# Optimization experiments

Hardware: AMD Instinct MI355X
Metric: run time of the kernel (lower is better)

## Reference

```python
import jax, jax.numpy as jnp
import numpy as np

M = 7          # window size
SHIFT = 3      # window_size // 2 (shift=True)
NUM_HEADS = 4


def _relative_position_index(m):
    coords = np.stack(np.meshgrid(np.arange(m), np.arange(m), indexing='ij')).reshape(2, -1)
    rel = (coords[:, :, None] - coords[:, None, :]).transpose(1, 2, 0).copy()  # (N,N,2)
    rel[..., 0] += m - 1
    rel[..., 1] += m - 1
    rel[..., 0] *= 2 * m - 1
    return rel.sum(-1).astype(np.int32)  # (N,N)


def _shift_attn_mask(H, W, m, s):
    img = np.zeros((H, W), np.float32)
    cnt = 0
    for hs in (slice(0, -m), slice(-m, -s), slice(-s, None)):
        for ws in (slice(0, -m), slice(-m, -s), slice(-s, None)):
            img[hs, ws] = cnt
            cnt += 1
    mw = img.reshape(H // m, m, W // m, m).transpose(0, 2, 1, 3).reshape(-1, m * m)  # (nW, N)
    diff = mw[:, None, :] - mw[:, :, None]
    return np.where(diff != 0, np.float32(-100.0), np.float32(0.0))  # (nW, N, N)


def setup_inputs():
    key = jax.random.key(0)
    k0, k1, k2, k3 = jax.random.split(key, 4)
    B, C, H, W = 32, 128, 112, 112
    h = NUM_HEADS
    x = jax.random.normal(k0, (B, C, H, W), jnp.float32)
    norm_w = jnp.ones((C,), jnp.float32)
    norm_b = jnp.zeros((C,), jnp.float32)
    qkv_w = jax.random.normal(k1, (3 * C, C), jnp.float32) * 0.02
    qkv_b = jnp.zeros((3 * C,), jnp.float32)
    proj_w = jax.random.normal(k2, (C, C), jnp.float32) * 0.02
    proj_b = jnp.zeros((C,), jnp.float32)
    bias_table = jax.random.normal(k3, ((2 * M - 1) ** 2, h), jnp.float32) * 0.02
    rel_index = jnp.asarray(_relative_position_index(M))
    attn_mask = jnp.asarray(_shift_attn_mask(H, W, M, SHIFT))
    return dict(x=x, norm_w=norm_w, norm_b=norm_b, qkv_w=qkv_w, qkv_b=qkv_b,
                proj_w=proj_w, proj_b=proj_b, bias_table=bias_table,
                rel_index=rel_index, attn_mask=attn_mask)


def reference(x, norm_w, norm_b, qkv_w, qkv_b, proj_w, proj_b, bias_table, rel_index, attn_mask):
    B, C, H, W = x.shape
    h = bias_table.shape[1]
    d = C // h
    N = M * M
    nH, nW = H // M, W // M

    xp = jnp.transpose(x, (0, 2, 3, 1))  # (B,H,W,C)
    shortcut = xp
    mu = xp.mean(-1, keepdims=True)
    var = ((xp - mu) ** 2).mean(-1, keepdims=True)
    xn = (xp - mu) / jnp.sqrt(var + 1e-5) * norm_w + norm_b

    xn = jnp.roll(xn, (-SHIFT, -SHIFT), (1, 2))  # cyclic shift

    # window partition -> (B*nH*nW, N, C)
    w = xn.reshape(B, nH, M, nW, M, C).transpose((0, 1, 3, 2, 4, 5)).reshape(-1, N, C)

    qkv = w @ qkv_w.T + qkv_b  # (B_, N, 3C)
    qkv = qkv.reshape(-1, N, 3, h, d).transpose((2, 0, 3, 1, 4))  # (3, B_, h, N, d)
    q, k, v = qkv[0], qkv[1], qkv[2]

    attn = jnp.einsum('bhnd,bhmd->bhnm', q, k) * (d ** -0.5)  # (B_, h, N, N)
    bias = bias_table[rel_index.reshape(-1)].reshape(N, N, h).transpose((2, 0, 1))  # (h,N,N)
    attn = attn + bias[None]

    nWnd = attn_mask.shape[0]  # number of windows per image
    attn = attn.reshape(B, nWnd, h, N, N) + attn_mask[None, :, None]
    attn = attn.reshape(-1, h, N, N)

    p = jax.nn.softmax(attn, axis=-1)
    o = jnp.einsum('bhnm,bhmd->bhnd', p, v).transpose((0, 2, 1, 3)).reshape(-1, N, C)
    o = o @ proj_w.T + proj_b

    # window reverse -> (B,H,W,C)
    o = o.reshape(B, nH, nW, M, M, C).transpose((0, 1, 3, 2, 4, 5)).reshape(B, H, W, C)
    o = jnp.roll(o, (SHIFT, SHIFT), (1, 2))  # reverse shift

    return jnp.transpose(shortcut + o, (0, 3, 1, 2))  # (B,C,H,W)
```

## Files before the change

### kernel.cpp

```cpp
#include <hip/hip_runtime.h>
#include <hip/hip_bf16.h>

typedef __attribute__((ext_vector_type(8))) short bf16x8;
typedef __attribute__((ext_vector_type(4))) float f32x4;
typedef __attribute__((ext_vector_type(8))) unsigned short ushort8;

__device__ __forceinline__ float bf2f(unsigned short u) {
  union { unsigned int i; float f; } v; v.i = ((unsigned int)u) << 16; return v.f;
}
__device__ __forceinline__ unsigned short f2bf(float f) {
  __hip_bfloat16 h = __float2bfloat16(f);
  unsigned short u; __builtin_memcpy(&u, &h, 2); return u;
}

__global__ void k_prep(const float* __restrict__ qkvw, const float* __restrict__ projw,
                       unsigned short* __restrict__ qkvw_bf,
                       unsigned short* __restrict__ projw_bf) {
  int t = blockIdx.x * 256 + threadIdx.x;
  int i = t * 4;
  const float* src;
  unsigned short* dst;
  int idx;
  if (i < 49152) { src = qkvw; dst = qkvw_bf; idx = i; }
  else           { src = projw; dst = projw_bf; idx = i - 49152; }
  float4 v = *(const float4*)(src + idx);
  union { unsigned short u[4]; uint2 v2; } o;
  o.u[0] = f2bf(v.x); o.u[1] = f2bf(v.y); o.u[2] = f2bf(v.z); o.u[3] = f2bf(v.w);
  *(uint2*)(dst + idx) = o.v2;
}

__global__ void k_bias(const float* __restrict__ bt,
                       const int* __restrict__ ri,
                       float* __restrict__ bp) {
  int t = blockIdx.x * 256 + threadIdx.x;
  int hq = t >> 12;
  int q  = (t >> 6) & 63;
  int k  = t & 63;
  float v = -1e30f;
  if (q < 49 && k < 49) v = bt[ri[q * 49 + k] * 4 + hq];
  bp[t] = v;
}

__global__ void k_mask(const float* __restrict__ am, float* __restrict__ mp) {
  int t = blockIdx.x * 256 + threadIdx.x;
  int w = t >> 12;
  int q = (t >> 6) & 63;
  int k = t & 63;
  float v = -1e30f;
  if (q < 49 && k < 49) v = am[w * 2401 + q * 49 + k];
  mp[t] = v;
}

__global__ __launch_bounds__(256, 3) void k_ln(const float* __restrict__ x,
                                               const float* __restrict__ nw,
                                               const float* __restrict__ nb,
                                               unsigned short* __restrict__ xw) {
  int p = blockIdx.x * 256 + threadIdx.x;
  int b = p / 12544;
  int r = p - b * 12544;
  int hh = r / 112;
  int wp = r - hh * 112;
  const float* bx = x + (size_t)b * 1605632 + r;

  float v[128];
  float s0 = 0.f, s1 = 0.f, q0 = 0.f, q1 = 0.f;
  #pragma unroll
  for (int c = 0; c < 128; c += 2) {
    float a = bx[(size_t)c * 12544];
    float bb = bx[(size_t)(c + 1) * 12544];
    v[c] = a; v[c + 1] = bb;
    s0 += a; q0 += a * a;
    s1 += bb; q1 += bb * bb;
  }
  float mu = (s0 + s1) * 0.0078125f;
  float var = (q0 + q1) * 0.0078125f - mu * mu;
  float rstd = rsqrtf(var + 1e-5f);

  int h2 = hh + 109; if (h2 >= 112) h2 -= 112;
  int w2 = wp + 109; if (w2 >= 112) w2 -= 112;
  int wh = h2 / 7, ii = h2 - wh * 7;
  int ww = w2 / 7, jj = w2 - ww * 7;
  int winl = (b * 16 + wh) * 16 + ww;
  unsigned short* dst = xw + ((size_t)winl * 49 + ii * 7 + jj) * 128;

  #pragma unroll
  for (int g = 0; g < 4; ++g) {
    unsigned int pk[16];
    #pragma unroll
    for (int q = 0; q < 16; ++q) {
      int c = g * 32 + 2 * q;
      float y0 = (v[c] - mu) * rstd * nw[c]         + nb[c];
      float y1 = (v[c + 1] - mu) * rstd * nw[c + 1] + nb[c + 1];
      pk[q] = (unsigned int)f2bf(y0) | ((unsigned int)f2bf(y1) << 16);
    }
    uint4* d4 = (uint4*)(dst + g * 32);
    #pragma unroll
    for (int k = 0; k < 4; ++k)
      d4[k] = make_uint4(pk[4 * k], pk[4 * k + 1], pk[4 * k + 2], pk[4 * k + 3]);
  }
}

__global__ __launch_bounds__(256, 3) void k_attn(
    const unsigned short* __restrict__ xw,
    const unsigned short* __restrict__ qkvw,
    const float* __restrict__ qkvb,
    const unsigned short* __restrict__ projw,
    const float* __restrict__ projb,
    const float* __restrict__ biasp,
    const float* __restrict__ maskp,
    unsigned short* __restrict__ yw) {
  __shared__ __attribute__((aligned(16))) char smem[49152];
  const int tid  = threadIdx.x;
  const int lane = tid & 63;
  const int h    = tid >> 6;
  const int m15  = lane & 15;
  const int quad = lane >> 4;
  const int win  = blockIdx.x;
  const int b    = win >> 8;
  const int wrem = win & 255;
  const int wh   = wrem >> 4;
  const int ww   = wrem & 15;
  const f32x4 fz = {0.f, 0.f, 0.f, 0.f};

  {
    const uint4* gsrc = (const uint4*)(xw + (size_t)win * 6272);
    #pragma unroll
    for (int it = 0; it < 4; ++it) {
      int cc = tid + it * 256;
      int row = cc >> 4, col = cc & 15;
      uint4 v = make_uint4(0u, 0u, 0u, 0u);
      if (cc < 784) v = gsrc[cc];
      *(uint4*)(smem + row * 256 + ((col ^ (row & 7)) << 4)) = v;
    }
  }
  __syncthreads();

  bf16x8 xf[4][4];
  #pragma unroll
  for (int mt = 0; mt < 4; ++mt) {
    int row = mt * 16 + m15;
    #pragma unroll
    for (int kt = 0; kt < 4; ++kt)
      xf[mt][kt] = *(const bf16x8*)(smem + row * 256 + (((kt * 4 + quad) ^ (row & 7)) << 4));
  }
  __syncthreads();

  char* const hb  = smem + h * 12288;
  char* const qpb = hb;
  char* const kpb = hb + 4096;
  char* const vpb = hb + 8192;

  #pragma unroll
  for (int g = 0; g < 2; ++g) {
    char* const dst = g ? kpb : qpb;
    #pragma unroll
    for (int sp = 0; sp < 2; ++sp) {
      int nt = g * 8 + 2 * h + sp;
      bf16x8 wfr[4];
      #pragma unroll
      for (int kt = 0; kt < 4; ++kt)
        wfr[kt] = *(const bf16x8*)(qkvw + (nt * 16 + m15) * 128 + kt * 32 + quad * 8);
      float4 b4 = *(const float4*)(qkvb + nt * 16 + quad * 4);
      #pragma unroll
      for (int mt = 0; mt < 4; ++mt) {
        f32x4 acc = fz;
        #pragma unroll
        for (int kt = 0; kt < 4; ++kt)
          acc = __builtin_amdgcn_mfma_f32_16x16x32_bf16(wfr[kt], xf[mt][kt], acc, 0, 0, 0);
        int row = mt * 16 + m15;
        union { unsigned short u[4]; uint2 v2; } o;
        o.u[0] = f2bf(acc[0] + b4.x); o.u[1] = f2bf(acc[1] + b4.y);
        o.u[2] = f2bf(acc[2] + b4.z); o.u[3] = f2bf(acc[3] + b4.w);
        int chunk = sp * 2 + (quad >> 1);
        *(uint2*)(dst + row * 64 + ((chunk ^ ((row >> 1) & 3)) << 4) + (quad & 1) * 8) = o.v2;
      }
    }
  }
  #pragma unroll
  for (int sp = 0; sp < 2; ++sp) {
    int nt = 16 + 2 * h + sp;
    bf16x8 wfr[4];
    #pragma unroll
    for (int kt = 0; kt < 4; ++kt)
      wfr[kt] = *(const bf16x8*)(qkvw + (nt * 16 + m15) * 128 + kt * 32 + quad * 8);
    float bias = qkvb[nt * 16 + m15];
    int dsub = sp * 16 + m15;
    #pragma unroll
    for (int mt = 0; mt < 4; ++mt) {
      f32x4 acc = fz;
      #pragma unroll
      for (int kt = 0; kt < 4; ++kt)
        acc = __builtin_amdgcn_mfma_f32_16x16x32_bf16(xf[mt][kt], wfr[kt], acc, 0, 0, 0);
      union { unsigned short u[4]; uint2 v2; } o;
      #pragma unroll
      for (int rr = 0; rr < 4; ++rr) o.u[rr] = f2bf(acc[rr] + bias);
      int chunk = mt * 2 + (quad >> 1);
      *(uint2*)(vpb + dsub * 128 + ((chunk ^ (dsub & 7)) << 4) + (quad & 1) * 8) = o.v2;
    }
  }

  bf16x8 qf[4], kf[4];
  #pragma unroll
  for (int t = 0; t < 4; ++t) {
    int row = t * 16 + m15;
    int sw = ((row >> 1) & 3) << 4;
    qf[t] = *(const bf16x8*)(qpb + row * 64 + ((quad << 4) ^ sw));
    kf[t] = *(const bf16x8*)(kpb + row * 64 + ((quad << 4) ^ sw));
  }
  f32x4 st[4][4];
  #pragma unroll
  for (int nt = 0; nt < 4; ++nt)
    #pragma unroll
    for (int mt = 0; mt < 4; ++mt)
      st[nt][mt] = __builtin_amdgcn_mfma_f32_16x16x32_bf16(kf[nt], qf[mt], fz, 0, 0, 0);

  const float* bp = biasp + h * 4096;
  const float* mp = maskp + wrem * 4096;
  #pragma unroll
  for (int mt = 0; mt < 4; ++mt) {
    int q = mt * 16 + m15;
    float sv[16];
    #pragma unroll
    for (int nt = 0; nt < 4; ++nt) {
      float4 bb = *(const float4*)(bp + q * 64 + nt * 16 + quad * 4);
      float4 mm = *(const float4*)(mp + q * 64 + nt * 16 + quad * 4);
      sv[nt * 4 + 0] = st[nt][mt][0] * 0.17677669529663687f + bb.x + mm.x;
      sv[nt * 4 + 1] = st[nt][mt][1] * 0.17677669529663687f + bb.y + mm.y;
      sv[nt * 4 + 2] = st[nt][mt][2] * 0.17677669529663687f + bb.z + mm.z;
      sv[nt * 4 + 3] = st[nt][mt][3] * 0.17677669529663687f + bb.w + mm.w;
    }
    float mx = sv[0];
    #pragma unroll
    for (int j = 1; j < 16; ++j) mx = fmaxf(mx, sv[j]);
    mx = fmaxf(mx, __shfl_xor(mx, 16));
    mx = fmaxf(mx, __shfl_xor(mx, 32));
    float sum = 0.f;
    #pragma unroll
    for (int j = 0; j < 16; ++j) { sv[j] = __expf(sv[j] - mx); sum += sv[j]; }
    sum += __shfl_xor(sum, 16);
    sum += __shfl_xor(sum, 32);
    float rinv = 1.0f / sum;
    #pragma unroll
    for (int nt = 0; nt < 4; ++nt) {
      union { unsigned short u[4]; uint2 v2; } o;
      #pragma unroll
      for (int rr = 0; rr < 4; ++rr) o.u[rr] = f2bf(sv[nt * 4 + rr] * rinv);
      int chunk = nt * 2 + (quad >> 1);
      *(uint2*)(qpb + q * 128 + ((chunk ^ (m15 & 7)) << 4) + (quad & 1) * 8) = o.v2;
    }
  }

  #pragma unroll
  for (int tt = 0; tt < 4; ++tt) {
    bf16x8 pf[2];
    #pragma unroll
    for (int kt = 0; kt < 2; ++kt) {
      int row = tt * 16 + m15;
      pf[kt] = *(const bf16x8*)(qpb + row * 128 + (((kt * 4 + quad) ^ (m15 & 7)) << 4));
    }
    #pragma unroll
    for (int dt = 0; dt < 2; ++dt) {
      f32x4 acc = fz;
      #pragma unroll
      for (int kt = 0; kt < 2; ++kt) {
        bf16x8 vf = *(const bf16x8*)(vpb + (dt * 16 + m15) * 128 + (((kt * 4 + quad) ^ (m15 & 7)) << 4));
        acc = __builtin_amdgcn_mfma_f32_16x16x32_bf16(vf, pf[kt], acc, 0, 0, 0);
      }
      int row = tt * 16 + m15;
      union { unsigned short u[4]; uint2 v2; } o;
      #pragma unroll
      for (int rr = 0; rr < 4; ++rr) o.u[rr] = f2bf(acc[rr]);
      int chunk = dt * 2 + (quad >> 1);
      *(uint2*)(qpb + row * 64 + ((chunk ^ ((row >> 1) & 3)) << 4) + (quad & 1) * 8) = o.v2;
    }
  }
  __syncthreads();

  bf16x8 of[4][4];
  #pragma unroll
  for (int mt = 0; mt < 4; ++mt) {
    int row = mt * 16 + m15;
    int sw = ((row >> 1) & 3) << 4;
    #pragma unroll
    for (int kt = 0; kt < 4; ++kt)
      of[mt][kt] = *(const bf16x8*)(smem + kt * 12288 + row * 64 + ((quad << 4) ^ sw));
  }
  int pixo[4];
  #pragma unroll
  for (int mt = 0; mt < 4; ++mt) {
    int token = mt * 16 + m15;
    int ii = token / 7, jj = token - ii * 7;
    int gh = wh * 7 + ii + 3; if (gh >= 112) gh -= 112;
    int gw = ww * 7 + jj + 3; if (gw >= 112) gw -= 112;
    pixo[mt] = gh * 112 + gw;
  }
  const size_t obase = (size_t)b * 1605632;
  #pragma unroll
  for (int sp = 0; sp < 2; ++sp) {
    int ct = 2 * h + sp;
    bf16x8 wf[4];
    #pragma unroll
    for (int kt = 0; kt < 4; ++kt)
      wf[kt] = *(const bf16x8*)(projw + (ct * 16 + m15) * 128 + kt * 32 + quad * 8);
    float4 pb4 = *(const float4*)(projb + ct * 16 + quad * 4);
    #pragma unroll
    for (int mt = 0; mt < 4; ++mt) {
      f32x4 acc = fz;
      #pragma unroll
      for (int kt = 0; kt < 4; ++kt)
        acc = __builtin_amdgcn_mfma_f32_16x16x32_bf16(wf[kt], of[mt][kt], acc, 0, 0, 0);
      int token = mt * 16 + m15;
      if (token < 49) {
        union { unsigned short u[4]; uint2 v2; } o;
        o.u[0] = f2bf(acc[0] + pb4.x); o.u[1] = f2bf(acc[1] + pb4.y);
        o.u[2] = f2bf(acc[2] + pb4.z); o.u[3] = f2bf(acc[3] + pb4.w);
        *(uint2*)(yw + obase + (size_t)pixo[mt] * 128 + ct * 16 + quad * 4) = o.v2;
      }
    }
  }
}

__global__ __launch_bounds__(256) void k_out(const unsigned short* __restrict__ yws,
                                             const float* __restrict__ x,
                                             float* __restrict__ out) {
  __shared__ __attribute__((aligned(16))) char T[28928];
  int tid = threadIdx.x;
  int bid = blockIdx.x;
  int b = bid / 112;
  int hh = bid - b * 112;
  const unsigned short* src = yws + (size_t)(b * 112 + hh) * 14336;
  #pragma unroll
  for (int it = 0; it < 7; ++it) {
    int cc = tid + it * 256;
    int w = cc >> 4, ci = cc & 15;
    *(uint4*)(T + ci * 1808 + w * 16) = *(const uint4*)(src + w * 128 + ci * 8);
  }
  __syncthreads();
  int c = tid >> 1, half = tid & 1;
  const char* tr = T + (c >> 3) * 1808 + (c & 7) * 2;
  size_t rowoff = ((size_t)(b * 128 + c) * 112 + hh) * 112;
  const float* xr = x + rowoff;
  float* outr = out + rowoff;
  #pragma unroll
  for (int s2 = 0; s2 < 7; ++s2) {
    int w = half * 56 + s2 * 8;
    float4 xa = *(const float4*)(xr + w);
    float4 xb = *(const float4*)(xr + w + 4);
    float4 oa, ob;
    oa.x = bf2f(*(const unsigned short*)(tr + (w + 0) * 16)) + xa.x;
    oa.y = bf2f(*(const unsigned short*)(tr + (w + 1) * 16)) + xa.y;
    oa.z = bf2f(*(const unsigned short*)(tr + (w + 2) * 16)) + xa.z;
    oa.w = bf2f(*(const unsigned short*)(tr + (w + 3) * 16)) + xa.w;
    ob.x = bf2f(*(const unsigned short*)(tr + (w + 4) * 16)) + xb.x;
    ob.y = bf2f(*(const unsigned short*)(tr + (w + 5) * 16)) + xb.y;
    ob.z = bf2f(*(const unsigned short*)(tr + (w + 6) * 16)) + xb.z;
    ob.w = bf2f(*(const unsigned short*)(tr + (w + 7) * 16)) + xb.w;
    *(float4*)(outr + w) = oa;
    *(float4*)(outr + w + 4) = ob;
  }
}

extern "C" void kernel_launch(void* const* d_in, const int* in_sizes, int n_in,
                              void* d_out, int out_size, void* d_ws, size_t ws_size,
                              hipStream_t stream) {
  const float* x     = (const float*)d_in[0];
  const float* nw    = (const float*)d_in[1];
  const float* nb    = (const float*)d_in[2];
  const float* qkvw  = (const float*)d_in[3];
  const float* qkvb  = (const float*)d_in[4];
  const float* projw = (const float*)d_in[5];
  const float* projb = (const float*)d_in[6];
  const float* bt    = (const float*)d_in[7];
  const int*   ri    = (const int*)d_in[8];
  const float* am    = (const float*)d_in[9];

  unsigned short* xw   = (unsigned short*)d_ws;
  unsigned short* yws  = (unsigned short*)((char*)d_ws + 102760448);
  float*          bp   = (float*)((char*)d_ws + 205520896);
  float*          mp   = (float*)((char*)d_ws + 205586432);
  unsigned short* qwbf = (unsigned short*)((char*)d_ws + 209780736);
  unsigned short* pwbf = (unsigned short*)((char*)d_ws + 209879040);
  float* out = (float*)d_out;

  k_prep<<<64,   256, 0, stream>>>(qkvw, projw, qwbf, pwbf);
  k_bias<<<64,   256, 0, stream>>>(bt, ri, bp);
  k_mask<<<4096, 256, 0, stream>>>(am, mp);
  k_ln  <<<1568, 256, 0, stream>>>(x, nw, nb, xw);
  k_attn<<<8192, 256, 0, stream>>>(xw, qwbf, qkvb, pwbf, projb, bp, mp, yws);
  k_out <<<3584, 256, 0, stream>>>(yws, x, out);
}
```

Before: 848.9 us.

## Keep Q/K/P in registers via 16x16x16 MFMA and shrink LDS footprint

New measurement: 891.8 us. +5.1%, slower.

```diff
diff --git a/kernel.cpp b/kernel.cpp
--- a/kernel.cpp
+++ b/kernel.cpp
@@ -2,6 +2,7 @@
 #include <hip/hip_bf16.h>
 
 typedef __attribute__((ext_vector_type(8))) short bf16x8;
+typedef __attribute__((ext_vector_type(4))) short bf16x4;
 typedef __attribute__((ext_vector_type(4))) float f32x4;
 typedef __attribute__((ext_vector_type(8))) unsigned short ushort8;
 
@@ -11,6 +12,19 @@
 __device__ __forceinline__ unsigned short f2bf(float f) {
   __hip_bfloat16 h = __float2bfloat16(f);
   unsigned short u; __builtin_memcpy(&u, &h, 2); return u;
+}
+__device__ __forceinline__ unsigned int pk2(float a, float b) {
+  return (unsigned int)f2bf(a) | ((unsigned int)f2bf(b) << 16);
+}
+
+__device__ __forceinline__ f32x4 mfma16(bf16x4 a, bf16x4 b, f32x4 c) {
+#if __has_builtin(__builtin_amdgcn_mfma_f32_16x16x16bf16_1k)
+  return __builtin_amdgcn_mfma_f32_16x16x16bf16_1k(a, b, c, 0, 0, 0);
+#else
+  asm volatile("v_mfma_f32_16x16x16_bf16 %0, %1, %2, %0\n\ts_nop 7\n\ts_nop 7"
+               : "+v"(c) : "v"(a), "v"(b));
+  return c;
+#endif
 }
 
 __global__ void k_prep(const float* __restrict__ qkvw, const float* __restrict__ projw,
@@ -51,7 +65,7 @@
   mp[t] = v;
 }
 
-__global__ __launch_bounds__(256, 3) void k_ln(const float* __restrict__ x,
+__global__ __launch_bounds__(256, 4) void k_ln(const float* __restrict__ x,
                                                const float* __restrict__ nw,
                                                const float* __restrict__ nb,
                                                unsigned short* __restrict__ xw) {
@@ -62,18 +76,14 @@
   int wp = r - hh * 112;
   const float* bx = x + (size_t)b * 1605632 + r;
 
-  float v[128];
-  float s0 = 0.f, s1 = 0.f, q0 = 0.f, q1 = 0.f;
-  #pragma unroll
-  for (int c = 0; c < 128; c += 2) {
-    float a = bx[(size_t)c * 12544];
-    float bb = bx[(size_t)(c + 1) * 12544];
-    v[c] = a; v[c + 1] = bb;
-    s0 += a; q0 += a * a;
-    s1 += bb; q1 += bb * bb;
-  }
-  float mu = (s0 + s1) * 0.0078125f;
-  float var = (q0 + q1) * 0.0078125f - mu * mu;
+  float sum = 0.f, ss = 0.f;
+  #pragma unroll 16
+  for (int c = 0; c < 128; ++c) {
+    float v = bx[(size_t)c * 12544];
+    sum += v; ss += v * v;
+  }
+  float mu = sum * 0.0078125f;
+  float var = ss * 0.0078125f - mu * mu;
   float rstd = rsqrtf(var + 1e-5f);
 
   int h2 = hh + 109; if (h2 >= 112) h2 -= 112;
@@ -89,8 +99,10 @@
     #pragma unroll
     for (int q = 0; q < 16; ++q) {
       int c = g * 32 + 2 * q;
-      float y0 = (v[c] - mu) * rstd * nw[c]         + nb[c];
-      float y1 = (v[c + 1] - mu) * rstd * nw[c + 1] + nb[c + 1];
+      float v0 = bx[(size_t)c * 12544];
+      float v1 = bx[(size_t)(c + 1) * 12544];
+      float y0 = (v0 - mu) * rstd * nw[c]     + nb[c];
+      float y1 = (v1 - mu) * rstd * nw[c + 1] + nb[c + 1];
       pk[q] = (unsigned int)f2bf(y0) | ((unsigned int)f2bf(y1) << 16);
     }
     uint4* d4 = (uint4*)(dst + g * 32);
@@ -100,7 +112,7 @@
   }
 }
 
-__global__ __launch_bounds__(256, 3) void k_attn(
+__global__ __launch_bounds__(256, 4) void k_attn(
     const unsigned short* __restrict__ xw,
     const unsigned short* __restrict__ qkvw,
     const float* __restrict__ qkvb,
@@ -109,7 +121,7 @@
     const float* __restrict__ biasp,
     const float* __restrict__ maskp,
     unsigned short* __restrict__ yw) {
-  __shared__ __attribute__((aligned(16))) char smem[49152];
+  __shared__ __attribute__((aligned(16))) char smem[32768];
   const int tid  = threadIdx.x;
   const int lane = tid & 63;
   const int h    = tid >> 6;
@@ -135,99 +147,85 @@
   }
   __syncthreads();
 
-  bf16x8 xf[4][4];
-  #pragma unroll
-  for (int mt = 0; mt < 4; ++mt) {
-    int row = mt * 16 + m15;
-    #pragma unroll
-    for (int kt = 0; kt < 4; ++kt)
-      xf[mt][kt] = *(const bf16x8*)(smem + row * 256 + (((kt * 4 + quad) ^ (row & 7)) << 4));
-  }
-  __syncthreads();
-
-  char* const hb  = smem + h * 12288;
-  char* const qpb = hb;
-  char* const kpb = hb + 4096;
-  char* const vpb = hb + 8192;
-
-  #pragma unroll
-  for (int g = 0; g < 2; ++g) {
-    char* const dst = g ? kpb : qpb;
+  char* const vpb = smem + 16384 + h * 4096;
+
+  bf16x4 qq[2][4], kk[2][4];
+  #pragma unroll
+  for (int mh = 0; mh < 2; ++mh) {
+    bf16x8 xf[2][4];
+    #pragma unroll
+    for (int m2 = 0; m2 < 2; ++m2) {
+      int row = (mh * 2 + m2) * 16 + m15;
+      #pragma unroll
+      for (int kt = 0; kt < 4; ++kt)
+        xf[m2][kt] = *(const bf16x8*)(smem + row * 256 + (((kt * 4 + quad) ^ (row & 7)) << 4));
+    }
+    #pragma unroll
+    for (int g = 0; g < 2; ++g) {
+      #pragma unroll
+      for (int sp = 0; sp < 2; ++sp) {
+        int nt = g * 8 + 2 * h + sp;
+        bf16x8 wfr[4];
+        #pragma unroll
+        for (int kt = 0; kt < 4; ++kt)
+          wfr[kt] = *(const bf16x8*)(qkvw + (nt * 16 + m15) * 128 + kt * 32 + quad * 8);
+        float4 b4 = *(const float4*)(qkvb + nt * 16 + quad * 4);
+        #pragma unroll
+        for (int m2 = 0; m2 < 2; ++m2) {
+          int mt = mh * 2 + m2;
+          f32x4 acc = fz;
+          #pragma unroll
+          for (int kt = 0; kt < 4; ++kt)
+            acc = __builtin_amdgcn_mfma_f32_16x16x32_bf16(wfr[kt], xf[m2][kt], acc, 0, 0, 0);
+          union { unsigned int u[2]; bf16x4 v; } pk;
+          pk.u[0] = pk2(acc[0] + b4.x, acc[1] + b4.y);
+          pk.u[1] = pk2(acc[2] + b4.z, acc[3] + b4.w);
+          if (g) kk[sp][mt] = pk.v; else qq[sp][mt] = pk.v;
+        }
+      }
+    }
     #pragma unroll
     for (int sp = 0; sp < 2; ++sp) {
-      int nt = g * 8 + 2 * h + sp;
+      int nt = 16 + 2 * h + sp;
       bf16x8 wfr[4];
       #pragma unroll
       for (int kt = 0; kt < 4; ++kt)
         wfr[kt] = *(const bf16x8*)(qkvw + (nt * 16 + m15) * 128 + kt * 32 + quad * 8);
-      float4 b4 = *(const float4*)(qkvb + nt * 16 + quad * 4);
-      #pragma unroll
-      for (int mt = 0; mt < 4; ++mt) {
+      float bias = qkvb[nt * 16 + m15];
+      int dsub = sp * 16 + m15;
+      #pragma unroll
+      for (int m2 = 0; m2 < 2; ++m2) {
+        int mt = mh * 2 + m2;
         f32x4 acc = fz;
         #pragma unroll
         for (int kt = 0; kt < 4; ++kt)
-          acc = __builtin_amdgcn_mfma_f32_16x16x32_bf16(wfr[kt], xf[mt][kt], acc, 0, 0, 0);
-        int row = mt * 16 + m15;
-        union { unsigned short u[4]; uint2 v2; } o;
-        o.u[0] = f2bf(acc[0] + b4.x); o.u[1] = f2bf(acc[1] + b4.y);
-        o.u[2] = f2bf(acc[2] + b4.z); o.u[3] = f2bf(acc[3] + b4.w);
-        int chunk = sp * 2 + (quad >> 1);
-        *(uint2*)(dst + row * 64 + ((chunk ^ ((row >> 1) & 3)) << 4) + (quad & 1) * 8) = o.v2;
+          acc = __builtin_amdgcn_mfma_f32_16x16x32_bf16(xf[m2][kt], wfr[kt], acc, 0, 0, 0);
+        uint2 o;
+        o.x = pk2(acc[0] + bias, acc[1] + bias);
+        o.y = pk2(acc[2] + bias, acc[3] + bias);
+        int chunk = mt * 2 + (quad >> 1);
+        *(uint2*)(vpb + dsub * 128 + ((chunk ^ (dsub & 7)) << 4) + (quad & 1) * 8) = o;
       }
     }
   }
-  #pragma unroll
-  for (int sp = 0; sp < 2; ++sp) {
-    int nt = 16 + 2 * h + sp;
-    bf16x8 wfr[4];
-    #pragma unroll
-    for (int kt = 0; kt < 4; ++kt)
-      wfr[kt] = *(const bf16x8*)(qkvw + (nt * 16 + m15) * 128 + kt * 32 + quad * 8);
-    float bias = qkvb[nt * 16 + m15];
-    int dsub = sp * 16 + m15;
-    #pragma unroll
-    for (int mt = 0; mt < 4; ++mt) {
-      f32x4 acc = fz;
-      #pragma unroll
-      for (int kt = 0; kt < 4; ++kt)
-        acc = __builtin_amdgcn_mfma_f32_16x16x32_bf16(xf[mt][kt], wfr[kt], acc, 0, 0, 0);
-      union { unsigned short u[4]; uint2 v2; } o;
-      #pragma unroll
-      for (int rr = 0; rr < 4; ++rr) o.u[rr] = f2bf(acc[rr] + bias);
-      int chunk = mt * 2 + (quad >> 1);
-      *(uint2*)(vpb + dsub * 128 + ((chunk ^ (dsub & 7)) << 4) + (quad & 1) * 8) = o.v2;
-    }
-  }
-
-  bf16x8 qf[4], kf[4];
-  #pragma unroll
-  for (int t = 0; t < 4; ++t) {
-    int row = t * 16 + m15;
-    int sw = ((row >> 1) & 3) << 4;
-    qf[t] = *(const bf16x8*)(qpb + row * 64 + ((quad << 4) ^ sw));
-    kf[t] = *(const bf16x8*)(kpb + row * 64 + ((quad << 4) ^ sw));
-  }
-  f32x4 st[4][4];
-  #pragma unroll
-  for (int nt = 0; nt < 4; ++nt)
-    #pragma unroll
-    for (int mt = 0; mt < 4; ++mt)
-      st[nt][mt] = __builtin_amdgcn_mfma_f32_16x16x32_bf16(kf[nt], qf[mt], fz, 0, 0, 0);
-
-  const float* bp = biasp + h * 4096;
-  const float* mp = maskp + wrem * 4096;
+
+  bf16x4 pp[4][4];
+  const float* bp_ = biasp + h * 4096;
+  const float* mp_ = maskp + wrem * 4096;
   #pragma unroll
   for (int mt = 0; mt < 4; ++mt) {
     int q = mt * 16 + m15;
     float sv[16];
     #pragma unroll
     for (int nt = 0; nt < 4; ++nt) {
-      float4 bb = *(const float4*)(bp + q * 64 + nt * 16 + quad * 4);
-      float4 mm = *(const float4*)(mp + q * 64 + nt * 16 + quad * 4);
-      sv[nt * 4 + 0] = st[nt][mt][0] * 0.17677669529663687f + bb.x + mm.x;
-      sv[nt * 4 + 1] = st[nt][mt][1] * 0.17677669529663687f + bb.y + mm.y;
-      sv[nt * 4 + 2] = st[nt][mt][2] * 0.17677669529663687f + bb.z + mm.z;
-      sv[nt * 4 + 3] = st[nt][mt][3] * 0.17677669529663687f + bb.w + mm.w;
+      f32x4 s = mfma16(kk[0][nt], qq[0][mt], fz);
+      s = mfma16(kk[1][nt], qq[1][mt], s);
+      float4 bb = *(const float4*)(bp_ + q * 64 + nt * 16 + quad * 4);
+      float4 mm = *(const float4*)(mp_ + q * 64 + nt * 16 + quad * 4);
+      sv[nt * 4 + 0] = s[0] * 0.17677669529663687f + bb.x + mm.x;
+      sv[nt * 4 + 1] = s[1] * 0.17677669529663687f + bb.y + mm.y;
+      sv[nt * 4 + 2] = s[2] * 0.17677669529663687f + bb.z + mm.z;
+      sv[nt * 4 + 3] = s[3] * 0.17677669529663687f + bb.w + mm.w;
     }
     float mx = sv[0];
     #pragma unroll
@@ -242,38 +240,45 @@
     float rinv = 1.0f / sum;
     #pragma unroll
     for (int nt = 0; nt < 4; ++nt) {
-      union { unsigned short u[4]; uint2 v2; } o;
-      #pragma unroll
-      for (int rr = 0; rr < 4; ++rr) o.u[rr] = f2bf(sv[nt * 4 + rr] * rinv);
-      int chunk = nt * 2 + (quad >> 1);
-      *(uint2*)(qpb + q * 128 + ((chunk ^ (m15 & 7)) << 4) + (quad & 1) * 8) = o.v2;
-    }
-  }
-
-  #pragma unroll
-  for (int tt = 0; tt < 4; ++tt) {
-    bf16x8 pf[2];
-    #pragma unroll
-    for (int kt = 0; kt < 2; ++kt) {
-      int row = tt * 16 + m15;
-      pf[kt] = *(const bf16x8*)(qpb + row * 128 + (((kt * 4 + quad) ^ (m15 & 7)) << 4));
-    }
+      union { unsigned int u[2]; bf16x4 v; } pk;
+      pk.u[0] = pk2(sv[nt * 4 + 0] * rinv, sv[nt * 4 + 1] * rinv);
+      pk.u[1] = pk2(sv[nt * 4 + 2] * rinv, sv[nt * 4 + 3] * rinv);
+      pp[mt][nt] = pk.v;
+    }
+  }
+
+  bf16x4 vf4[4][2];
+  #pragma unroll
+  for (int nt = 0; nt < 4; ++nt)
+    #pragma unroll
+    for (int dt = 0; dt < 2; ++dt) {
+      int r = dt * 16 + m15;
+      union { uint2 u; bf16x4 v; } ld;
+      ld.u = *(const uint2*)(vpb + r * 128 + (((nt * 2 + (quad >> 1)) ^ (r & 7)) << 4) + (quad & 1) * 8);
+      vf4[nt][dt] = ld.v;
+    }
+  f32x4 oacc[4][2];
+  #pragma unroll
+  for (int tt = 0; tt < 4; ++tt)
     #pragma unroll
     for (int dt = 0; dt < 2; ++dt) {
       f32x4 acc = fz;
       #pragma unroll
-      for (int kt = 0; kt < 2; ++kt) {
-        bf16x8 vf = *(const bf16x8*)(vpb + (dt * 16 + m15) * 128 + (((kt * 4 + quad) ^ (m15 & 7)) << 4));
-        acc = __builtin_amdgcn_mfma_f32_16x16x32_bf16(vf, pf[kt], acc, 0, 0, 0);
-      }
+      for (int nt = 0; nt < 4; ++nt)
+        acc = mfma16(vf4[nt][dt], pp[tt][nt], acc);
+      oacc[tt][dt] = acc;
+    }
+  #pragma unroll
+  for (int tt = 0; tt < 4; ++tt)
+    #pragma unroll
+    for (int dt = 0; dt < 2; ++dt) {
       int row = tt * 16 + m15;
-      union { unsigned short u[4]; uint2 v2; } o;
-      #pragma unroll
-      for (int rr = 0; rr < 4; ++rr) o.u[rr] = f2bf(acc[rr]);
+      uint2 o;
+      o.x = pk2(oacc[tt][dt][0], oacc[tt][dt][1]);
+      o.y = pk2(oacc[tt][dt][2], oacc[tt][dt][3]);
       int chunk = dt * 2 + (quad >> 1);
-      *(uint2*)(qpb + row * 64 + ((chunk ^ ((row >> 1) & 3)) << 4) + (quad & 1) * 8) = o.v2;
-    }
-  }
+      *(uint2*)(vpb + row * 64 + ((chunk ^ ((row >> 1) & 3)) << 4) + (quad & 1) * 8) = o;
+    }
   __syncthreads();
 
   bf16x8 of[4][4];
@@ -283,7 +288,7 @@
     int sw = ((row >> 1) & 3) << 4;
     #pragma unroll
     for (int kt = 0; kt < 4; ++kt)
-      of[mt][kt] = *(const bf16x8*)(smem + kt * 12288 + row * 64 + ((quad << 4) ^ sw));
+      of[mt][kt] = *(const bf16x8*)(smem + 16384 + kt * 4096 + row * 64 + ((quad << 4) ^ sw));
   }
   int pixo[4];
   #pragma unroll
```
